# Optimization experiments

Measured on AMD Instinct MI355X. Metric: run time of the kernel, lower is better.

The kernel has to match this reference:

```python
import jax, jax.numpy as jnp
import numpy as np
from jax import lax

BETA = 0.3

def setup_inputs() -> dict:
    key = jax.random.key(0)
    ks = jax.random.split(key, 5)
    B, C, H, W = 1, 64, 96, 96
    x = jax.random.normal(ks[0], (B, C, H, W), dtype=jnp.float32)
    # d_conv: Conv2d(C, C, k=3, stride=1, padding=2, dilation=2)
    dW = jax.random.normal(ks[1], (C, C, 3, 3), dtype=jnp.float32) * 0.05
    db = jax.random.normal(ks[2], (C,), dtype=jnp.float32) * 0.05
    # conv: Conv2d(C, C, k=1)
    cW = jax.random.normal(ks[3], (C, C, 1, 1), dtype=jnp.float32) * 0.1
    cb = jax.random.normal(ks[4], (C,), dtype=jnp.float32) * 0.05
    return {"x": x, "dW": dW, "db": db, "cW": cW, "cb": cb}

def _conv(x, w, b, padding, dilation):
    y = lax.conv_general_dilated(
        x, w, window_strides=(1, 1),
        padding=[(padding, padding), (padding, padding)],
        rhs_dilation=(dilation, dilation),
        dimension_numbers=("NCHW", "OIHW", "NCHW"))
    return y + b[None, :, None, None]

def reference(x, dW, db, cW, cb):
    B, C, H, W = x.shape
    HW = H * W
    y = _conv(x, dW, db, padding=2, dilation=2)   # (B,C,H,W), same d_conv used for q and k
    v = _conv(x, cW, cb, padding=0, dilation=1).reshape(B, HW, C)
    # NOTE: torch uses raw .reshape (not transpose) for q — faithful here.
    q = y.reshape(B, HW, C)
    k = y.reshape(B, C, HW)
    qk = jnp.einsum("bnc,bcm->bnm", q, k)         # (B,HW,HW)
    qk = jnp.where(jnp.abs(qk) > BETA, qk, 0.0)   # threshold mask (qk*mask)
    att = jax.nn.softmax(qk, axis=-1)
    att = jnp.einsum("bnm,bmc->bnc", att, v)      # (B,HW,C)
    att = att.swapaxes(1, 2).reshape(B, C, H, W)
    return x + att
```

## Files before the change

kernel.cpp:

```cpp
#include <hip/hip_runtime.h>
#include <hip/hip_bf16.h>

#define CC 64
#define HW 9216
#define IMG 96
#define PW 100
#define SPLITS 8
#define SPLEN 1152
#define ITERS 18
#define LOG2E 1.44269504f

typedef _Float16 f16;
typedef __attribute__((ext_vector_type(8))) _Float16 f16x8;
typedef __attribute__((ext_vector_type(4))) _Float16 f16x4;
typedef __attribute__((ext_vector_type(2))) _Float16 f16x2;
typedef __attribute__((ext_vector_type(4))) float f32x4;

__global__ __launch_bounds__(256) void prepad_kernel(
    const float* __restrict__ x, f16* __restrict__ xpad)
{
    int i = blockIdx.x * 256 + threadIdx.x;
    if (i >= CC * PW * PW) return;
    int ci = i / (PW * PW), p = i % (PW * PW);
    int r = p / PW, c = p % PW;
    bool inside = (r >= 2 && r < IMG + 2 && c >= 2 && c < IMG + 2);
    float v = inside ? x[ci * HW + (r - 2) * IMG + (c - 2)] : 0.f;
    xpad[i] = (f16)v;
}

__global__ __launch_bounds__(256) void conv_dil_kernel(
    const f16* __restrict__ xpad, const float* __restrict__ dW, const float* __restrict__ db,
    const float* __restrict__ cW, const float* __restrict__ cb,
    f16* __restrict__ yq, f16* __restrict__ kt, f16* __restrict__ vt)
{
    const int co = blockIdx.x / 18, chunk = blockIdx.x % 18;
    const int t = threadIdx.x;
    const int m0 = chunk * 512 + 2 * t;
    const int h = m0 / IMG, w = m0 % IMG;
    const int pbase = h * PW + w;
    const float* wco = dW + co * 576;
    const float* cwo = cW + co * CC;

    float a0, a1, v0, v1;
    a0 = a1 = db[co];
    v0 = v1 = cb[co];
    #pragma unroll 2
    for (int ci = 0; ci < CC; ++ci) {
        const f16* rp0 = xpad + ci * (PW * PW) + pbase;
        const float* wk = wco + ci * 9;
        const float cw = cwo[ci];
        #pragma unroll
        for (int kh = 0; kh < 3; ++kh) {
            const f16* rp = rp0 + kh * (2 * PW);
            f16x2 A = *(const f16x2*)(rp);
            f16x2 B = *(const f16x2*)(rp + 2);
            f16x2 C = *(const f16x2*)(rp + 4);
            float e0 = (float)A.x, e1 = (float)A.y;
            float e2 = (float)B.x, e3 = (float)B.y;
            float e4 = (float)C.x, e5 = (float)C.y;
            float w0 = wk[kh * 3 + 0], w1 = wk[kh * 3 + 1], w2 = wk[kh * 3 + 2];
            a0 += w0 * e0 + w1 * e2 + w2 * e4;
            a1 += w0 * e1 + w1 * e3 + w2 * e5;
            if (kh == 1) {
                v0 += cw * e2; v1 += cw * e3;
            }
        }
    }
    f16 h0 = (f16)a0, h1 = (f16)a1;
    *(f16x2*)&yq[co * HW + m0] = (f16x2){h0, h1};
    kt[(m0 + 0) * 64 + co] = h0;
    kt[(m0 + 1) * 64 + co] = h1;
    vt[((m0 + 0) & 63) * HW + co * 144 + ((m0 + 0) >> 6)] = (f16)v0;
    vt[((m0 + 1) & 63) * HW + co * 144 + ((m0 + 1) >> 6)] = (f16)v1;
}

__global__ __launch_bounds__(256, 4) void attn_kernel(
    const f16* __restrict__ kt, const f16* __restrict__ vt, const f16* __restrict__ yq,
    f16* __restrict__ acc_ws, float* __restrict__ m_ws, float* __restrict__ l_ws)
{
    __shared__ f16 sKT[64 * 72];
    __shared__ f16 sVT[64 * 72];
    __shared__ f16 sPS[4 * 16 * 72];
    __shared__ float sAL[4 * 16];

    const int t = threadIdx.x;
    const int L = t & 63, w = t >> 6;
    const int g = L >> 4, c16 = L & 15;
    const int qb = blockIdx.x >> 3, sp = blockIdx.x & 7;
    const int n0 = qb * 64;
    const int mbase = sp * SPLEN;
    f16* psw = (f16*)sPS + w * 16 * 72;

    f16x8 qa[2];
    #pragma unroll
    for (int kc = 0; kc < 2; ++kc)
        qa[kc] = *(const f16x8*)(yq + (n0 + w * 16 + c16) * 64 + g * 8 + kc * 32);

    float mi = -1e30f;
    float li = 0.f;
    f32x4 acc[4];
    #pragma unroll
    for (int ct = 0; ct < 4; ++ct) acc[ct] = (f32x4){0.f, 0.f, 0.f, 0.f};

    for (int it = 0; it < ITERS; ++it) {
        const int m0 = mbase + it * 64;
        __syncthreads();
        #pragma unroll
        for (int rep = 0; rep < 2; ++rep) {
            int idx = t + rep * 256;
            int row = idx >> 3, ch = idx & 7;
            *(uint4*)&sKT[row * 72 + ch * 8] = *(const uint4*)&kt[(m0 + row) * 64 + ch * 8];
            *(uint4*)&sVT[row * 72 + ch * 8] = *(const uint4*)&vt[row * HW + m0 + ch * 8];
        }
        __syncthreads();

        f32x4 s[4];
        #pragma unroll
        for (int mt = 0; mt < 4; ++mt) {
            f32x4 a0 = (f32x4){0.f, 0.f, 0.f, 0.f};
            #pragma unroll
            for (int kc = 0; kc < 2; ++kc) {
                f16x8 kb = *(const f16x8*)&sKT[(mt * 16 + c16) * 72 + g * 8 + kc * 32];
                a0 = __builtin_amdgcn_mfma_f32_16x16x32_f16(kb, qa[kc], a0, 0, 0, 0);
            }
            s[mt] = a0;
        }
        #pragma unroll
        for (int mt = 0; mt < 4; ++mt)
            #pragma unroll
            for (int j = 0; j < 4; ++j)
                s[mt][j] = (fabsf(s[mt][j]) > 0.3f) ? s[mt][j] : 0.f;

        float x0 = fmaxf(fmaxf(s[0][0], s[0][1]), fmaxf(s[0][2], s[0][3]));
        float x1 = fmaxf(fmaxf(s[1][0], s[1][1]), fmaxf(s[1][2], s[1][3]));
        float x2 = fmaxf(fmaxf(s[2][0], s[2][1]), fmaxf(s[2][2], s[2][3]));
        float x3 = fmaxf(fmaxf(s[3][0], s[3][1]), fmaxf(s[3][2], s[3][3]));
        float mx = fmaxf(fmaxf(x0, x1), fmaxf(x2, x3));
        mx = fmaxf(mx, __shfl_xor(mx, 16, 64));
        mx = fmaxf(mx, __shfl_xor(mx, 32, 64));
        float mnew = fmaxf(mi, mx);
        float nL = mnew * LOG2E;
        float alpha = __builtin_amdgcn_exp2f(mi * LOG2E - nL);
        mi = mnew;

        float p[16];
        #pragma unroll
        for (int mt = 0; mt < 4; ++mt)
            #pragma unroll
            for (int j = 0; j < 4; ++j)
                p[mt * 4 + j] = __builtin_amdgcn_exp2f(fmaf(s[mt][j], LOG2E, -nL));
        float q0 = (p[0] + p[1]) + (p[2] + p[3]);
        float q1 = (p[4] + p[5]) + (p[6] + p[7]);
        float q2 = (p[8] + p[9]) + (p[10] + p[11]);
        float q3 = (p[12] + p[13]) + (p[14] + p[15]);
        li = li * alpha + ((q0 + q1) + (q2 + q3));

        #pragma unroll
        for (int mt = 0; mt < 4; ++mt) {
            unsigned u0 = __builtin_bit_cast(unsigned int,
                __builtin_amdgcn_cvt_pkrtz(p[mt * 4 + 0], p[mt * 4 + 1]));
            unsigned u1 = __builtin_bit_cast(unsigned int,
                __builtin_amdgcn_cvt_pkrtz(p[mt * 4 + 2], p[mt * 4 + 3]));
            uint2 uv; uv.x = u0; uv.y = u1;
            *(uint2*)&psw[c16 * 72 + mt * 16 + 4 * g] = uv;
        }

        if (g == 0) sAL[w * 16 + c16] = alpha;
        f32x4 aj = *(const f32x4*)&sAL[w * 16 + 4 * g];
        #pragma unroll
        for (int ct = 0; ct < 4; ++ct)
            #pragma unroll
            for (int j = 0; j < 4; ++j) acc[ct][j] *= aj[j];

        f16x8 pa[2];
        #pragma unroll
        for (int kc = 0; kc < 2; ++kc)
            pa[kc] = *(const f16x8*)&psw[c16 * 72 + g * 8 + kc * 32];
        #pragma unroll
        for (int ct = 0; ct < 4; ++ct)
            #pragma unroll
            for (int kc = 0; kc < 2; ++kc) {
                f16x8 vb = *(const f16x8*)&sVT[(ct * 16 + c16) * 72 + g * 8 + kc * 32];
                acc[ct] = __builtin_amdgcn_mfma_f32_16x16x32_f16(pa[kc], vb, acc[ct], 0, 0, 0);
            }
    }

    float li_tot = li;
    li_tot += __shfl_xor(li_tot, 16, 64);
    li_tot += __shfl_xor(li_tot, 32, 64);

    const int base = blockIdx.x;
    #pragma unroll
    for (int ct = 0; ct < 4; ++ct)
        #pragma unroll
        for (int j = 0; j < 4; ++j)
            acc_ws[base * 4096 + (w * 16 + 4 * g + j) * 64 + ct * 16 + c16] = (f16)acc[ct][j];
    if (g == 0) {
        m_ws[base * 64 + w * 16 + c16] = mi;
        l_ws[base * 64 + w * 16 + c16] = li_tot;
    }
}

__global__ __launch_bounds__(256) void merge_kernel(
    const f16* __restrict__ acc_ws, const float* __restrict__ m_ws, const float* __restrict__ l_ws,
    const float* __restrict__ x, float* __restrict__ out)
{
    __shared__ float wsh[SPLITS * 16];
    __shared__ float att[64 * 17];
    const int qb = blockIdx.x >> 2, sub = blockIdx.x & 3;
    const int r0 = sub * 16;
    const int t = threadIdx.x;
    if (t < 16) {
        int row = r0 + t;
        float ms = -1e30f;
        float mv[SPLITS];
        #pragma unroll
        for (int sp = 0; sp < SPLITS; ++sp) {
            mv[sp] = m_ws[(qb * SPLITS + sp) * 64 + row];
            ms = fmaxf(ms, mv[sp]);
        }
        float Lsum = 0.f, ev[SPLITS];
        #pragma unroll
        for (int sp = 0; sp < SPLITS; ++sp) {
            ev[sp] = __builtin_amdgcn_exp2f((mv[sp] - ms) * LOG2E);
            Lsum += l_ws[(qb * SPLITS + sp) * 64 + row] * ev[sp];
        }
        float inv = 1.f / Lsum;
        #pragma unroll
        for (int sp = 0; sp < SPLITS; ++sp)
            wsh[sp * 16 + t] = ev[sp] * inv;
    }
    __syncthreads();
    for (int i = t; i < 1024; i += 256) {
        int rr = i >> 6, c = i & 63;
        float v = 0.f;
        #pragma unroll
        for (int sp = 0; sp < SPLITS; ++sp)
            v += (float)acc_ws[(qb * SPLITS + sp) * 4096 + (r0 + rr) * 64 + c] * wsh[sp * 16 + rr];
        att[c * 17 + rr] = v;
    }
    __syncthreads();
    const int n0 = qb * 64 + r0;
    for (int i = t; i < 1024; i += 256) {
        int c = i >> 4, r = i & 15;
        int idx = c * HW + n0 + r;
        out[idx] = x[idx] + att[c * 17 + r];
    }
}

extern "C" void kernel_launch(void* const* d_in, const int* in_sizes, int n_in,
                              void* d_out, int out_size, void* d_ws, size_t ws_size,
                              hipStream_t stream)
{
    const float* x  = (const float*)d_in[0];
    const float* dW = (const float*)d_in[1];
    const float* db = (const float*)d_in[2];
    const float* cW = (const float*)d_in[3];
    const float* cb = (const float*)d_in[4];
    float* out = (float*)d_out;

    char* ws = (char*)d_ws;
    f16* kt     = (f16*)(ws);
    f16* yq     = (f16*)(ws + 1179648);
    f16* vt     = (f16*)(ws + 2359296);
    f16* xpad   = (f16*)(ws + 3538944);
    f16* acc_ws = (f16*)(ws + 4818944);
    float* m_ws = (float*)(ws + 14256128);
    float* l_ws = (float*)(ws + 14551040);

    prepad_kernel<<<dim3((CC * PW * PW + 255) / 256), dim3(256), 0, stream>>>(x, xpad);
    conv_dil_kernel<<<dim3(64 * 18), dim3(256), 0, stream>>>(xpad, dW, db, cW, cb, yq, kt, vt);
    attn_kernel<<<dim3(144 * SPLITS), dim3(256), 0, stream>>>(kt, vt, yq, acc_ws, m_ws, l_ws);
    merge_kernel<<<dim3(576), dim3(256), 0, stream>>>(acc_ws, m_ws, l_ws, x, out);
}
```

Before: 159.1 us.

## Compute dilated and pointwise convolutions with MFMA on channels-last padded input

Replaces the scalar per-output-channel dilated 3x3 conv with an implicit-GEMM version using 16x16x32 f16 MFMA instructions. Weights are staged in LDS as f16 per tap, and the 1x1 conv is folded in at the center tap. The prepad kernel now transposes the input into a channels-last padded f16 layout via an LDS tile, so each tap reads contiguous channel vectors. This is meant to cut the conv's scalar FMA cost; the outputs stay in the same layouts, though kt/vt stores remain scattered.

Result: faster. 141.7 us (-10.9%).

```diff
diff --git a/kernel.cpp b/kernel.cpp
--- a/kernel.cpp
+++ b/kernel.cpp
@@ -4,7 +4,6 @@
 #define CC 64
 #define HW 9216
 #define IMG 96
-#define PW 100
 #define SPLITS 8
 #define SPLEN 1152
 #define ITERS 18
@@ -17,61 +16,107 @@
 typedef __attribute__((ext_vector_type(4))) float f32x4;
 
 __global__ __launch_bounds__(256) void prepad_kernel(
-    const float* __restrict__ x, f16* __restrict__ xpad)
-{
-    int i = blockIdx.x * 256 + threadIdx.x;
-    if (i >= CC * PW * PW) return;
-    int ci = i / (PW * PW), p = i % (PW * PW);
-    int r = p / PW, c = p % PW;
-    bool inside = (r >= 2 && r < IMG + 2 && c >= 2 && c < IMG + 2);
-    float v = inside ? x[ci * HW + (r - 2) * IMG + (c - 2)] : 0.f;
-    xpad[i] = (f16)v;
-}
-
-__global__ __launch_bounds__(256) void conv_dil_kernel(
-    const f16* __restrict__ xpad, const float* __restrict__ dW, const float* __restrict__ db,
+    const float* __restrict__ x, f16* __restrict__ xt)
+{
+    __shared__ float tile[64][65];
+    const int p0 = blockIdx.x * 64;
+    const int t = threadIdx.x;
+    const int pl = t & 63;
+    const int p = p0 + pl;
+    int r = p / 100, c = p % 100;
+    bool interior = (r >= 2) && (r < 98) && (c >= 2) && (c < 98);
+    int img = (r - 2) * IMG + (c - 2);
+    #pragma unroll
+    for (int j = 0; j < 16; ++j) {
+        int ci = j * 4 + (t >> 6);
+        tile[pl][ci] = interior ? x[ci * HW + img] : 0.f;
+    }
+    __syncthreads();
+    const int row16 = t >> 4, chunk = t & 15;
+    #pragma unroll
+    for (int j = 0; j < 4; ++j) {
+        int row = j * 16 + row16;
+        int pr = p0 + row;
+        if (pr < 10000) {
+            f16x4 hv = {(f16)tile[row][chunk * 4 + 0], (f16)tile[row][chunk * 4 + 1],
+                        (f16)tile[row][chunk * 4 + 2], (f16)tile[row][chunk * 4 + 3]};
+            *(f16x4*)&xt[pr * 64 + chunk * 4] = hv;
+        }
+    }
+}
+
+__global__ __launch_bounds__(256) void conv_mfma_kernel(
+    const f16* __restrict__ xt, const float* __restrict__ dW, const float* __restrict__ db,
     const float* __restrict__ cW, const float* __restrict__ cb,
     f16* __restrict__ yq, f16* __restrict__ kt, f16* __restrict__ vt)
 {
-    const int co = blockIdx.x / 18, chunk = blockIdx.x % 18;
+    __shared__ f16 Wl[9 * 16 * 64];
+    __shared__ f16 cWl[16 * 64];
+
+    const int b = blockIdx.x;
+    const int mblk = b >> 2, cog = b & 3;
+    const int co0 = cog * 16;
     const int t = threadIdx.x;
-    const int m0 = chunk * 512 + 2 * t;
-    const int h = m0 / IMG, w = m0 % IMG;
-    const int pbase = h * PW + w;
-    const float* wco = dW + co * 576;
-    const float* cwo = cW + co * CC;
-
-    float a0, a1, v0, v1;
-    a0 = a1 = db[co];
-    v0 = v1 = cb[co];
-    #pragma unroll 2
-    for (int ci = 0; ci < CC; ++ci) {
-        const f16* rp0 = xpad + ci * (PW * PW) + pbase;
-        const float* wk = wco + ci * 9;
-        const float cw = cwo[ci];
-        #pragma unroll
-        for (int kh = 0; kh < 3; ++kh) {
-            const f16* rp = rp0 + kh * (2 * PW);
-            f16x2 A = *(const f16x2*)(rp);
-            f16x2 B = *(const f16x2*)(rp + 2);
-            f16x2 C = *(const f16x2*)(rp + 4);
-            float e0 = (float)A.x, e1 = (float)A.y;
-            float e2 = (float)B.x, e3 = (float)B.y;
-            float e4 = (float)C.x, e5 = (float)C.y;
-            float w0 = wk[kh * 3 + 0], w1 = wk[kh * 3 + 1], w2 = wk[kh * 3 + 2];
-            a0 += w0 * e0 + w1 * e2 + w2 * e4;
-            a1 += w0 * e1 + w1 * e3 + w2 * e5;
-            if (kh == 1) {
-                v0 += cw * e2; v1 += cw * e3;
-            }
-        }
-    }
-    f16 h0 = (f16)a0, h1 = (f16)a1;
-    *(f16x2*)&yq[co * HW + m0] = (f16x2){h0, h1};
-    kt[(m0 + 0) * 64 + co] = h0;
-    kt[(m0 + 1) * 64 + co] = h1;
-    vt[((m0 + 0) & 63) * HW + co * 144 + ((m0 + 0) >> 6)] = (f16)v0;
-    vt[((m0 + 1) & 63) * HW + co * 144 + ((m0 + 1) >> 6)] = (f16)v1;
+
+    #pragma unroll 4
+    for (int j = 0; j < 36; ++j) {
+        int d = j * 256 + t;
+        int tap = d >> 10, rem = d & 1023, co = rem >> 6, ci = rem & 63;
+        Wl[d] = (f16)dW[(co0 + co) * 576 + ci * 9 + tap];
+    }
+    #pragma unroll
+    for (int j = 0; j < 4; ++j) {
+        int d = j * 256 + t;
+        cWl[d] = (f16)cW[(co0 + (d >> 6)) * CC + (d & 63)];
+    }
+    __syncthreads();
+
+    const int w = t >> 6, L = t & 63, g = L >> 4, c16 = L & 15;
+    const int ms = mblk * 64 + w * 16;
+    const int h = ms / IMG, wc = ms % IMG;
+    const int pb = (h + 2) * 100 + (wc + 2) + c16;
+
+    f16x8 Bf[9][2], Bv[2];
+    #pragma unroll
+    for (int tap = 0; tap < 9; ++tap)
+        #pragma unroll
+        for (int kc = 0; kc < 2; ++kc)
+            Bf[tap][kc] = *(const f16x8*)&Wl[(tap * 16 + c16) * 64 + g * 8 + kc * 32];
+    #pragma unroll
+    for (int kc = 0; kc < 2; ++kc)
+        Bv[kc] = *(const f16x8*)&cWl[c16 * 64 + g * 8 + kc * 32];
+
+    f32x4 accY = (f32x4){0.f, 0.f, 0.f, 0.f};
+    f32x4 accV = (f32x4){0.f, 0.f, 0.f, 0.f};
+
+    #pragma unroll
+    for (int tap = 0; tap < 9; ++tap) {
+        int kh = tap / 3, kw = tap % 3;
+        int toff = (2 * kh - 2) * 100 + (2 * kw - 2);
+        const f16* ap = xt + (pb + toff) * 64;
+        f16x8 A0 = *(const f16x8*)(ap + g * 8);
+        f16x8 A1 = *(const f16x8*)(ap + g * 8 + 32);
+        accY = __builtin_amdgcn_mfma_f32_16x16x32_f16(A0, Bf[tap][0], accY, 0, 0, 0);
+        accY = __builtin_amdgcn_mfma_f32_16x16x32_f16(A1, Bf[tap][1], accY, 0, 0, 0);
+        if (tap == 4) {
+            accV = __builtin_amdgcn_mfma_f32_16x16x32_f16(A0, Bv[0], accV, 0, 0, 0);
+            accV = __builtin_amdgcn_mfma_f32_16x16x32_f16(A1, Bv[1], accV, 0, 0, 0);
+        }
+    }
+
+    const float dbv = db[co0 + c16], cbv = cb[co0 + c16];
+    f16 hy[4];
+    #pragma unroll
+    for (int j = 0; j < 4; ++j) hy[j] = (f16)(accY[j] + dbv);
+    *(f16x4*)&yq[(co0 + c16) * HW + ms + 4 * g] = (f16x4){hy[0], hy[1], hy[2], hy[3]};
+    #pragma unroll
+    for (int j = 0; j < 4; ++j)
+        kt[(ms + 4 * g + j) * 64 + co0 + c16] = hy[j];
+    #pragma unroll
+    for (int j = 0; j < 4; ++j) {
+        int m = ms + 4 * g + j;
+        vt[(m & 63) * HW + (co0 + c16) * 144 + (m >> 6)] = (f16)(accV[j] + cbv);
+    }
 }
 
 __global__ __launch_bounds__(256, 4) void attn_kernel(
@@ -263,13 +308,13 @@
     f16* kt     = (f16*)(ws);
     f16* yq     = (f16*)(ws + 1179648);
     f16* vt     = (f16*)(ws + 2359296);
-    f16* xpad   = (f16*)(ws + 3538944);
+    f16* xt     = (f16*)(ws + 3538944);
     f16* acc_ws = (f16*)(ws + 4818944);
     float* m_ws = (float*)(ws + 14256128);
     float* l_ws = (float*)(ws + 14551040);
 
-    prepad_kernel<<<dim3((CC * PW * PW + 255) / 256), dim3(256), 0, stream>>>(x, xpad);
-    conv_dil_kernel<<<dim3(64 * 18), dim3(256), 0, stream>>>(xpad, dW, db, cW, cb, yq, kt, vt);
+    prepad_kernel<<<dim3(157), dim3(256), 0, stream>>>(x, xt);
+    conv_mfma_kernel<<<dim3(576), dim3(256), 0, stream>>>(xt, dW, db, cW, cb, yq, kt, vt);
     attn_kernel<<<dim3(144 * SPLITS), dim3(256), 0, stream>>>(kt, vt, yq, acc_ws, m_ws, l_ws);
     merge_kernel<<<dim3(576), dim3(256), 0, stream>>>(acc_ws, m_ws, l_ws, x, out);
 }
```
